# Kernel optimization log

Hardware: AMD Instinct MI355X
Metric: run time of the kernel (lower is better)

Reference implementation:

```python
import jax, jax.numpy as jnp
import numpy as np

D = 1024
H = 16
HD = D // H
EPS = 1e-5

def _layernorm(x, g, b):
    xf = x.astype(jnp.float32)
    mu = jnp.mean(xf, axis=-1, keepdims=True)
    var = jnp.mean(jnp.square(xf - mu), axis=-1, keepdims=True)
    return ((xf - mu) * jax.lax.rsqrt(var + EPS) * g + b).astype(x.dtype)

def setup_inputs() -> dict:
    key = jax.random.key(0)
    ks = jax.random.split(key, 12)
    B, S = 4, 1024
    s_in = 1.0 / np.sqrt(D)
    inp = {
        "x": jax.random.normal(ks[0], (B, S, D), dtype=jnp.float32),
        "in_proj_w": jax.random.normal(ks[1], (3 * D, D), dtype=jnp.float32) * s_in,
        "in_proj_b": jnp.zeros((3 * D,), dtype=jnp.float32),
        "out_w": jax.random.normal(ks[2], (D, D), dtype=jnp.float32) * s_in,
        "out_b": jnp.zeros((D,), dtype=jnp.float32),
        "ln1_g": jnp.ones((D,), dtype=jnp.float32),
        "ln1_b": jnp.zeros((D,), dtype=jnp.float32),
        "fc_w": jax.random.normal(ks[3], (4 * D, D), dtype=jnp.float32) * s_in,
        "fc_b": jnp.zeros((4 * D,), dtype=jnp.float32),
        "proj_w": jax.random.normal(ks[4], (D, 4 * D), dtype=jnp.float32) * (1.0 / np.sqrt(4 * D)),
        "proj_b": jnp.zeros((D,), dtype=jnp.float32),
        "ln2_g": jnp.ones((D,), dtype=jnp.float32),
        "ln2_b": jnp.zeros((D,), dtype=jnp.float32),
    }
    return inp

def reference(x, in_proj_w, in_proj_b, out_w, out_b, ln1_g, ln1_b,
              fc_w, fc_b, proj_w, proj_b, ln2_g, ln2_b):
    B, S, _ = x.shape
    scaling = float(HD) ** -0.5
    # --- attention sublayer ---
    h = _layernorm(x, ln1_g, ln1_b)
    qkv = h @ in_proj_w.T + in_proj_b              # [B,S,3D]
    q, k, v = jnp.split(qkv, 3, axis=-1)
    q = (q * scaling).reshape(B, S, H, HD).transpose(0, 2, 1, 3)  # [B,H,S,hd]
    k = k.reshape(B, S, H, HD).transpose(0, 2, 1, 3)
    v = v.reshape(B, S, H, HD).transpose(0, 2, 1, 3)
    attn = jax.nn.softmax(jnp.einsum('bhqd,bhkd->bhqk', q, k), axis=-1)
    o = jnp.einsum('bhqk,bhkd->bhqd', attn, v).transpose(0, 2, 1, 3).reshape(B, S, D)
    x = x + o @ out_w.T + out_b
    # --- MLP sublayer (QuickGELU) ---
    h = _layernorm(x, ln2_g, ln2_b)
    u = h @ fc_w.T + fc_b                          # [B,S,4D]
    u = u * jax.nn.sigmoid(1.702 * u)
    x = x + u @ proj_w.T + proj_b
    return x
```

## Files before the change

### kernel.cpp

```cpp
#include <hip/hip_runtime.h>
#include <math.h>

#define D_MODEL 1024
#define SEQ     1024
#define BATCH   4
#define NTOK    (BATCH * SEQ)

typedef __bf16 bf16;
using bfrag = __attribute__((ext_vector_type(8))) __bf16;
using ffrag = __attribute__((ext_vector_type(4))) float;

__device__ __forceinline__ ffrag mfma16(bfrag a, bfrag b, ffrag c) {
  return __builtin_amdgcn_mfma_f32_16x16x32_bf16(a, b, c, 0, 0, 0);
}

__device__ __forceinline__ void gload_lds16(const void* g, void* l) {
  __builtin_amdgcn_global_load_lds(
      (const __attribute__((address_space(1))) void*)g,
      (__attribute__((address_space(3))) void*)l, 16, 0, 0);
}

__device__ __forceinline__ int xcd_remap(int flat, int nwg) {
  return (flat & 7) * (nwg >> 3) + (flat >> 3);
}

__global__ void convert_all(const float* __restrict__ s0, bf16* __restrict__ d0, int n0,
                            const float* __restrict__ s1, bf16* __restrict__ d1, int n1,
                            const float* __restrict__ s2, bf16* __restrict__ d2, int n2,
                            const float* __restrict__ s3, bf16* __restrict__ d3, int n3,
                            float scale, int limit0) {
  const float* src; bf16* dst; int n; int limit = 0;
  switch (blockIdx.y) {
    case 0: src = s0; dst = d0; n = n0; limit = limit0; break;
    case 1: src = s1; dst = d1; n = n1; break;
    case 2: src = s2; dst = d2; n = n2; break;
    default: src = s3; dst = d3; n = n3; break;
  }
  int i = blockIdx.x * blockDim.x + threadIdx.x;
  const int stride = gridDim.x * blockDim.x;
  for (; i < n; i += stride) {
    float4 v = ((const float4*)src)[i];
    float sc = (i < limit) ? scale : 1.0f;
    bf16* d = dst + (size_t)i * 4;
    d[0] = (bf16)(v.x * sc); d[1] = (bf16)(v.y * sc);
    d[2] = (bf16)(v.z * sc); d[3] = (bf16)(v.w * sc);
  }
}

__global__ void scale_bias(const float* __restrict__ src, float* __restrict__ dst,
                           int n, int limit, float scale) {
  int i = blockIdx.x * blockDim.x + threadIdx.x;
  if (i < n) dst[i] = src[i] * (i < limit ? scale : 1.0f);
}

__global__ __launch_bounds__(256) void ln_row(const float* __restrict__ x,
                                              const float* __restrict__ gamma,
                                              const float* __restrict__ beta,
                                              bf16* __restrict__ out) {
  const int row = blockIdx.x, tid = threadIdx.x;
  const float4 v = ((const float4*)(x + (size_t)row * D_MODEL))[tid];
  float s  = v.x + v.y + v.z + v.w;
  float ss = v.x * v.x + v.y * v.y + v.z * v.z + v.w * v.w;
#pragma unroll
  for (int off = 32; off >= 1; off >>= 1) {
    s  += __shfl_xor(s, off);
    ss += __shfl_xor(ss, off);
  }
  __shared__ float rs[4], rss[4];
  const int w = tid >> 6;
  if ((tid & 63) == 0) { rs[w] = s; rss[w] = ss; }
  __syncthreads();
  s  = rs[0] + rs[1] + rs[2] + rs[3];
  ss = rss[0] + rss[1] + rss[2] + rss[3];
  const float mu   = s * (1.0f / D_MODEL);
  const float var  = ss * (1.0f / D_MODEL) - mu * mu;
  const float rstd = rsqrtf(var + 1e-5f);
  const float4 gv = ((const float4*)gamma)[tid];
  const float4 bv = ((const float4*)beta)[tid];
  bf16* o = out + (size_t)row * D_MODEL + tid * 4;
  o[0] = (bf16)((v.x - mu) * rstd * gv.x + bv.x);
  o[1] = (bf16)((v.y - mu) * rstd * gv.y + bv.y);
  o[2] = (bf16)((v.z - mu) * rstd * gv.z + bv.z);
  o[3] = (bf16)((v.w - mu) * rstd * gv.w + bv.w);
}

template <int EPI>
__global__ __launch_bounds__(256, 4) void gemm_bt(
    const bf16* __restrict__ A, const bf16* __restrict__ B,
    const float* __restrict__ bias, const float* __restrict__ resid,
    float* __restrict__ outF, bf16* __restrict__ outB,
    int M, int N, int K) {
  __shared__ bf16 As[2][128 * 32];
  __shared__ bf16 Bs[2][128 * 32];
  const int tid = threadIdx.x;
  const int lane = tid & 63, w = tid >> 6;
  const int wm = w >> 1, wn = w & 1;
  const int ql = lane & 15, lg = lane >> 4;
  const int nwg = gridDim.x * gridDim.y;
  const int flat = xcd_remap(blockIdx.y * gridDim.x + blockIdx.x, nwg);
  const int m0 = (flat % gridDim.x) * 128, n0 = (flat / gridDim.x) * 128;

  ffrag acc[4][4];
#pragma unroll
  for (int i = 0; i < 4; i++)
#pragma unroll
    for (int j = 0; j < 4; j++) acc[i][j] = ffrag{0.f, 0.f, 0.f, 0.f};

  const int r0 = tid >> 2;
  const int jsw = (tid & 3) ^ ((r0 >> 1) & 3);
  const bf16* a0 = A + (size_t)(m0 + r0) * K + jsw * 8;
  const bf16* a1 = A + (size_t)(m0 + 64 + r0) * K + jsw * 8;
  const bf16* b0 = B + (size_t)(n0 + r0) * K + jsw * 8;
  const bf16* b1 = B + (size_t)(n0 + 64 + r0) * K + jsw * 8;
  const int lo = w * 512;

  auto STAGE = [&](int bs, int kk) {
    gload_lds16(a0 + kk, &As[bs][lo]);
    gload_lds16(a1 + kk, &As[bs][2048 + lo]);
    gload_lds16(b0 + kk, &Bs[bs][lo]);
    gload_lds16(b1 + kk, &Bs[bs][2048 + lo]);
  };

  STAGE(0, 0);
  __syncthreads();

  int cur = 0;
  for (int k0 = 0; k0 < K; k0 += 32) {
    if (k0 + 32 < K) STAGE(cur ^ 1, k0 + 32);
    bfrag af[4], bfr[4];
#pragma unroll
    for (int i = 0; i < 4; i++) {
      const int row = wm * 64 + i * 16 + ql;
      af[i] = *(const bfrag*)&As[cur][row * 32 + ((lg ^ ((row >> 1) & 3)) * 8)];
    }
#pragma unroll
    for (int j = 0; j < 4; j++) {
      const int row = wn * 64 + j * 16 + ql;
      bfr[j] = *(const bfrag*)&Bs[cur][row * 32 + ((lg ^ ((row >> 1) & 3)) * 8)];
    }
#pragma unroll
    for (int i = 0; i < 4; i++)
#pragma unroll
      for (int j = 0; j < 4; j++)
        acc[i][j] = mfma16(af[i], bfr[j], acc[i][j]);
    __syncthreads();
    cur ^= 1;
  }

#pragma unroll
  for (int i = 0; i < 4; i++) {
    const int row = m0 + wm * 64 + i * 16 + lg * 4;
#pragma unroll
    for (int j = 0; j < 4; j++) {
      const int col = n0 + wn * 64 + j * 16 + ql;
      const float bv = bias[col];
#pragma unroll
      for (int r = 0; r < 4; r++) {
        float v = acc[i][j][r] + bv;
        const size_t idx = (size_t)(row + r) * N + col;
        if (EPI == 0) {
          outB[idx] = (bf16)v;
        } else if (EPI == 1) {
          outF[idx] = v + resid[idx];
        } else {
          outB[idx] = (bf16)(v / (1.0f + __expf(-1.702f * v)));
        }
      }
    }
  }
}

template <int EPI>
__global__ __launch_bounds__(256, 4) void gemm_bt64(
    const bf16* __restrict__ A, const bf16* __restrict__ B,
    const float* __restrict__ bias, const float* __restrict__ resid,
    float* __restrict__ outF, bf16* __restrict__ outB,
    int M, int N, int K) {
  __shared__ bf16 As[2][64 * 64];
  __shared__ bf16 Bs[2][64 * 64];
  const int tid = threadIdx.x;
  const int lane = tid & 63, w = tid >> 6;
  const int wm = w >> 1, wn = w & 1;
  const int ql = lane & 15, lg = lane >> 4;
  const int m0 = blockIdx.x * 64, n0 = blockIdx.y * 64;

  ffrag acc[2][2];
#pragma unroll
  for (int i = 0; i < 2; i++)
#pragma unroll
    for (int j = 0; j < 2; j++) acc[i][j] = ffrag{0.f, 0.f, 0.f, 0.f};

  const int r0 = tid >> 3;
  const int jsw = ((tid & 7) ^ (r0 & 7)) * 8;
  const bf16* a0 = A + (size_t)(m0 + r0) * K + jsw;
  const bf16* a1 = A + (size_t)(m0 + 32 + r0) * K + jsw;
  const bf16* b0 = B + (size_t)(n0 + r0) * K + jsw;
  const bf16* b1 = B + (size_t)(n0 + 32 + r0) * K + jsw;
  const int lo = tid * 8;

  auto STAGE = [&](int bs, int kk) {
    gload_lds16(a0 + kk, &As[bs][lo]);
    gload_lds16(a1 + kk, &As[bs][2048 + lo]);
    gload_lds16(b0 + kk, &Bs[bs][lo]);
    gload_lds16(b1 + kk, &Bs[bs][2048 + lo]);
  };

  STAGE(0, 0);
  __syncthreads();

  int cur = 0;
  for (int k0 = 0; k0 < K; k0 += 64) {
    if (k0 + 64 < K) STAGE(cur ^ 1, k0 + 64);
    bfrag af[2][2], bfr[2][2];
#pragma unroll
    for (int i = 0; i < 2; i++) {
      const int row = wm * 32 + i * 16 + ql;
      const int r7 = row & 7;
#pragma unroll
      for (int kc = 0; kc < 2; kc++)
        af[i][kc] = *(const bfrag*)&As[cur][row * 64 + (((lg + 4 * kc) ^ r7) * 8)];
    }
#pragma unroll
    for (int j = 0; j < 2; j++) {
      const int row = wn * 32 + j * 16 + ql;
      const int r7 = row & 7;
#pragma unroll
      for (int kc = 0; kc < 2; kc++)
        bfr[j][kc] = *(const bfrag*)&Bs[cur][row * 64 + (((lg + 4 * kc) ^ r7) * 8)];
    }
#pragma unroll
    for (int kc = 0; kc < 2; kc++)
#pragma unroll
      for (int i = 0; i < 2; i++)
#pragma unroll
        for (int j = 0; j < 2; j++)
          acc[i][j] = mfma16(af[i][kc], bfr[j][kc], acc[i][j]);
    __syncthreads();
    cur ^= 1;
  }

#pragma unroll
  for (int i = 0; i < 2; i++) {
    const int row = m0 + wm * 32 + i * 16 + lg * 4;
#pragma unroll
    for (int j = 0; j < 2; j++) {
      const int col = n0 + wn * 32 + j * 16 + ql;
      const float bv = bias[col];
#pragma unroll
      for (int r = 0; r < 4; r++) {
        float v = acc[i][j][r] + bv;
        const size_t idx = (size_t)(row + r) * N + col;
        if (EPI == 0) {
          outB[idx] = (bf16)v;
        } else if (EPI == 1) {
          outF[idx] = v + resid[idx];
        } else {
          outB[idx] = (bf16)(v / (1.0f + __expf(-1.702f * v)));
        }
      }
    }
  }
}

__global__ __launch_bounds__(256) void transpose_v(const bf16* __restrict__ qkv,
                                                   bf16* __restrict__ vt) {
  __shared__ bf16 T[64 * 66];
  const int tid = threadIdx.x;
  const int bh = blockIdx.y, b = bh >> 4, h = bh & 15;
  const int s0 = blockIdx.x * 64;
  const bf16* src = qkv + (size_t)b * SEQ * 3072 + 2048 + h * 64;

  const int sl = tid >> 3, c = tid & 7;
#pragma unroll
  for (int p = 0; p < 2; p++) {
    const int s = sl + p * 32;
    const bfrag v = *(const bfrag*)(src + (size_t)(s0 + s) * 3072 + c * 8);
#pragma unroll
    for (int e = 0; e < 8; e++) T[s * 66 + c * 8 + e] = v[e];
  }
  __syncthreads();
  bf16* dst = vt + (size_t)bh * 64 * 1024;
#pragma unroll
  for (int p = 0; p < 2; p++) {
    const int d = sl + p * 32;
    bfrag o;
#pragma unroll
    for (int e = 0; e < 8; e++) o[e] = T[(c * 8 + e) * 66 + d];
    *(bfrag*)(dst + (size_t)d * 1024 + s0 + c * 8) = o;
  }
}

__global__ __launch_bounds__(256, 3) void flash_attn(const bf16* __restrict__ qkv,
                                                     const bf16* __restrict__ vt,
                                                     bf16* __restrict__ o) {
  __shared__ bf16 Kl[128 * 64];
  __shared__ bf16 Vl[64 * 128];
  __shared__ bf16 Pl[4 * 16 * 136];
  const int tid = threadIdx.x, lane = tid & 63, wid = tid >> 6;
  const int ql = lane & 15, lg = lane >> 4;
  const int flat = xcd_remap(blockIdx.y * 16 + blockIdx.x, 1024);
  const int bh = flat >> 4, b = bh >> 4, h = bh & 15;
  const int qrow0 = (flat & 15) * 64 + wid * 16;
  const size_t headq = (size_t)b * SEQ * 3072 + (size_t)h * 64;

  const bf16* qp = qkv + headq + (size_t)(qrow0 + ql) * 3072 + lg * 8;
  const bfrag q0 = *(const bfrag*)qp;
  const bfrag q1 = *(const bfrag*)(qp + 32);

  float mrun[4], lrun[4];
  ffrag oacc[4];
#pragma unroll
  for (int r = 0; r < 4; r++) { mrun[r] = -1e30f; lrun[r] = 0.0f; }
#pragma unroll
  for (int f = 0; f < 4; f++) oacc[f] = ffrag{0.f, 0.f, 0.f, 0.f};

  const int kr0 = tid >> 3;
  const int kjsw = ((tid & 7) ^ (kr0 & 7)) * 8;
  const bf16* kp = qkv + headq + 1024 + (size_t)kr0 * 3072 + kjsw;
  const int vr_ = tid >> 4, vlc = tid & 15;
  const bf16* vhead = vt + (size_t)bh * 64 * 1024;
  bf16* Pw = Pl + wid * 2176;

  for (int kt = 0; kt < SEQ; kt += 128) {
#pragma unroll
    for (int pp = 0; pp < 4; pp++)
      gload_lds16(kp + (size_t)(kt + pp * 32) * 3072, &Kl[pp * 2048 + tid * 8]);
#pragma unroll
    for (int pp = 0; pp < 4; pp++) {
      const int vr = pp * 16 + vr_;
      const int gc = vlc ^ (vr & 7);
      gload_lds16(vhead + (size_t)vr * 1024 + kt + gc * 8, &Vl[(pp * 256 + tid) * 8]);
    }
    __syncthreads();

    ffrag sa[8];
    __builtin_amdgcn_s_setprio(1);
#pragma unroll
    for (int sub = 0; sub < 8; sub++) {
      const int krow = sub * 16 + ql;
      const int r7 = krow & 7;
      const bfrag kf0 = *(const bfrag*)&Kl[krow * 64 + ((lg ^ r7) * 8)];
      const bfrag kf1 = *(const bfrag*)&Kl[krow * 64 + (((lg + 4) ^ r7) * 8)];
      ffrag s4 = ffrag{0.f, 0.f, 0.f, 0.f};
      s4 = mfma16(q0, kf0, s4);
      s4 = mfma16(q1, kf1, s4);
      sa[sub] = s4;
    }
    __builtin_amdgcn_s_setprio(0);

    float lmax[4];
#pragma unroll
    for (int r = 0; r < 4; r++) {
      float m = sa[0][r];
#pragma unroll
      for (int sub = 1; sub < 8; sub++) m = fmaxf(m, sa[sub][r]);
      lmax[r] = m;
    }
    bool ok = (lmax[0] - mrun[0] <= 8.0f) && (lmax[1] - mrun[1] <= 8.0f) &&
              (lmax[2] - mrun[2] <= 8.0f) && (lmax[3] - mrun[3] <= 8.0f);
    if (!__all(ok)) {
#pragma unroll
      for (int r = 0; r < 4; r++) {
        float mx = lmax[r];
        mx = fmaxf(mx, __shfl_xor(mx, 1));
        mx = fmaxf(mx, __shfl_xor(mx, 2));
        mx = fmaxf(mx, __shfl_xor(mx, 4));
        mx = fmaxf(mx, __shfl_xor(mx, 8));
        const float mnew = fmaxf(mrun[r], mx);
        const float corr = exp2f(mrun[r] - mnew);
        lrun[r] *= corr;
#pragma unroll
        for (int f = 0; f < 4; f++) oacc[f][r] *= corr;
        mrun[r] = mnew;
      }
    }
#pragma unroll
    for (int r = 0; r < 4; r++) {
      float srow = 0.f;
      bf16* prow = Pw + (lg * 4 + r) * 136;
#pragma unroll
      for (int sub = 0; sub < 8; sub++) {
        const float pv = exp2f(sa[sub][r] - mrun[r]);
        srow += pv;
        prow[sub * 16 + ql] = (bf16)pv;
      }
      lrun[r] += srow;
    }

    bfrag pa[4];
#pragma unroll
    for (int kc = 0; kc < 4; kc++)
      pa[kc] = *(const bfrag*)&Pw[ql * 136 + kc * 32 + lg * 8];
    __builtin_amdgcn_s_setprio(1);
#pragma unroll
    for (int f = 0; f < 4; f++) {
      const int vrow = f * 16 + ql;
      const int r7 = vrow & 7;
#pragma unroll
      for (int kc = 0; kc < 4; kc++) {
        const bfrag vf = *(const bfrag*)&Vl[vrow * 128 + (((kc * 4 + lg) ^ r7) * 8)];
        oacc[f] = mfma16(pa[kc], vf, oacc[f]);
      }
    }
    __builtin_amdgcn_s_setprio(0);
    __syncthreads();
  }

  float rinv[4];
#pragma unroll
  for (int r = 0; r < 4; r++) {
    float ls = lrun[r];
    ls += __shfl_xor(ls, 1);
    ls += __shfl_xor(ls, 2);
    ls += __shfl_xor(ls, 4);
    ls += __shfl_xor(ls, 8);
    rinv[r] = 1.0f / ls;
  }
#pragma unroll
  for (int f = 0; f < 4; f++) {
#pragma unroll
    for (int r = 0; r < 4; r++) {
      const size_t orow = (size_t)b * SEQ + qrow0 + lg * 4 + r;
      o[orow * 1024 + h * 64 + f * 16 + ql] = (bf16)(oacc[f][r] * rinv[r]);
    }
  }
}

extern "C" void kernel_launch(void* const* d_in, const int* in_sizes, int n_in,
                              void* d_out, int out_size, void* d_ws, size_t ws_size,
                              hipStream_t stream) {
  (void)in_sizes; (void)n_in; (void)out_size; (void)ws_size;
  const float* x      = (const float*)d_in[0];
  const float* in_w   = (const float*)d_in[1];
  const float* in_b   = (const float*)d_in[2];
  const float* out_w  = (const float*)d_in[3];
  const float* out_b  = (const float*)d_in[4];
  const float* ln1_g  = (const float*)d_in[5];
  const float* ln1_b  = (const float*)d_in[6];
  const float* fc_w   = (const float*)d_in[7];
  const float* fc_b   = (const float*)d_in[8];
  const float* proj_w = (const float*)d_in[9];
  const float* proj_b = (const float*)d_in[10];
  const float* ln2_g  = (const float*)d_in[11];
  const float* ln2_b  = (const float*)d_in[12];
  float* out = (float*)d_out;

  char* p = (char*)d_ws;
  auto alloc = [&](size_t bytes) { char* r = p; p += (bytes + 255) & ~255ull; return r; };
  bf16* w_qkv  = (bf16*)alloc((size_t)3072 * 1024 * 2);
  bf16* w_out  = (bf16*)alloc((size_t)1024 * 1024 * 2);
  bf16* w_fc   = (bf16*)alloc((size_t)4096 * 1024 * 2);
  bf16* w_proj = (bf16*)alloc((size_t)1024 * 4096 * 2);
  float* b_qkv = (float*)alloc((size_t)3072 * 4);
  bf16* hbuf   = (bf16*)alloc((size_t)NTOK * 1024 * 2);
  float* x2    = (float*)alloc((size_t)NTOK * 1024 * 4);
  bf16* qkv    = (bf16*)alloc((size_t)NTOK * 3072 * 2);
  bf16* aout   = (bf16*)alloc((size_t)NTOK * 1024 * 2);
  bf16* ubuf   = qkv;
  bf16* vtb    = (bf16*)x2;

  const float scaling = 0.125f * 1.44269504089f;
  convert_all<<<dim3(1024, 4), 256, 0, stream>>>(
      in_w, w_qkv, 3072 * 1024 / 4,
      out_w, w_out, 1024 * 1024 / 4,
      fc_w, w_fc, 4096 * 1024 / 4,
      proj_w, w_proj, 4096 * 1024 / 4,
      scaling, 1024 * 1024 / 4);
  scale_bias<<<12, 256, 0, stream>>>(in_b, b_qkv, 3072, 1024, scaling);

  ln_row<<<NTOK, 256, 0, stream>>>(x, ln1_g, ln1_b, hbuf);
  gemm_bt<0><<<dim3(32, 24), 256, 0, stream>>>(hbuf, w_qkv, b_qkv, nullptr,
                                               nullptr, qkv, NTOK, 3072, 1024);
  transpose_v<<<dim3(16, 64), 256, 0, stream>>>(qkv, vtb);
  flash_attn<<<dim3(16, 64), 256, 0, stream>>>(qkv, vtb, aout);
  gemm_bt64<1><<<dim3(64, 16), 256, 0, stream>>>(aout, w_out, out_b, x,
                                                 x2, nullptr, NTOK, 1024, 1024);
  ln_row<<<NTOK, 256, 0, stream>>>(x2, ln2_g, ln2_b, hbuf);
  gemm_bt<2><<<dim3(32, 32), 256, 0, stream>>>(hbuf, w_fc, fc_b, nullptr,
                                               nullptr, ubuf, NTOK, 4096, 1024);
  gemm_bt64<1><<<dim3(64, 16), 256, 0, stream>>>(ubuf, w_proj, proj_b, x2,
                                                 out, nullptr, NTOK, 1024, 4096);
}
```

Before: 228.5 us.

## Rewrite flash attention with 32x32 MFMA, transposed scores and register-resident P

Flash attention now uses 32x32x16 bf16 MFMA, computing S^T as K·Q so that each lane owns a single query column. The softmax probabilities are packed to bf16 and exchanged between half-waves with shuffles, so P no longer takes a round trip through LDS. Each block now handles 128 query rows (32 per wave) instead of 64, which halves the grid and doubles K/V reuse per LDS load. Occupancy drops to 2 blocks per CU, and the rescale and normalise steps go through a small LDS broadcast buffer; the new swizzles and fragment mappings carry correctness risk.

```diff
diff --git a/kernel.cpp b/kernel.cpp
--- a/kernel.cpp
+++ b/kernel.cpp
@@ -7,11 +7,20 @@
 #define NTOK    (BATCH * SEQ)
 
 typedef __bf16 bf16;
-using bfrag = __attribute__((ext_vector_type(8))) __bf16;
-using ffrag = __attribute__((ext_vector_type(4))) float;
+using bfrag  = __attribute__((ext_vector_type(8))) __bf16;
+using ffrag  = __attribute__((ext_vector_type(4))) float;
+using f32x16 = __attribute__((ext_vector_type(16))) float;
 
 __device__ __forceinline__ ffrag mfma16(bfrag a, bfrag b, ffrag c) {
   return __builtin_amdgcn_mfma_f32_16x16x32_bf16(a, b, c, 0, 0, 0);
+}
+__device__ __forceinline__ f32x16 mfma32(bfrag a, bfrag b, f32x16 c) {
+  return __builtin_amdgcn_mfma_f32_32x32x16_bf16(a, b, c, 0, 0, 0);
+}
+__device__ __forceinline__ unsigned cvt_pk(float lo, float hi) {
+  unsigned r;
+  asm("v_cvt_pk_bf16_f32 %0, %1, %2" : "=v"(r) : "v"(lo), "v"(hi));
+  return r;
 }
 
 __device__ __forceinline__ void gload_lds16(const void* g, void* l) {
@@ -290,36 +299,33 @@
   }
 }
 
-__global__ __launch_bounds__(256, 3) void flash_attn(const bf16* __restrict__ qkv,
+__global__ __launch_bounds__(256, 2) void flash_attn(const bf16* __restrict__ qkv,
                                                      const bf16* __restrict__ vt,
                                                      bf16* __restrict__ o) {
   __shared__ bf16 Kl[128 * 64];
   __shared__ bf16 Vl[64 * 128];
-  __shared__ bf16 Pl[4 * 16 * 136];
+  __shared__ float RB[4][32];
   const int tid = threadIdx.x, lane = tid & 63, wid = tid >> 6;
-  const int ql = lane & 15, lg = lane >> 4;
-  const int flat = xcd_remap(blockIdx.y * 16 + blockIdx.x, 1024);
-  const int bh = flat >> 4, b = bh >> 4, h = bh & 15;
-  const int qrow0 = (flat & 15) * 64 + wid * 16;
+  const int l31 = lane & 31, hi = lane >> 5;
+  const int flat = xcd_remap(blockIdx.y * 8 + blockIdx.x, 512);
+  const int qblk = flat & 7, bh = flat >> 3, b = bh >> 4, h = bh & 15;
+  const int qb0 = qblk * 128 + wid * 32;
   const size_t headq = (size_t)b * SEQ * 3072 + (size_t)h * 64;
 
-  const bf16* qp = qkv + headq + (size_t)(qrow0 + ql) * 3072 + lg * 8;
-  const bfrag q0 = *(const bfrag*)qp;
-  const bfrag q1 = *(const bfrag*)(qp + 32);
-
-  float mrun[4], lrun[4];
-  ffrag oacc[4];
-#pragma unroll
-  for (int r = 0; r < 4; r++) { mrun[r] = -1e30f; lrun[r] = 0.0f; }
-#pragma unroll
-  for (int f = 0; f < 4; f++) oacc[f] = ffrag{0.f, 0.f, 0.f, 0.f};
-
-  const int kr0 = tid >> 3;
-  const int kjsw = ((tid & 7) ^ (kr0 & 7)) * 8;
-  const bf16* kp = qkv + headq + 1024 + (size_t)kr0 * 3072 + kjsw;
-  const int vr_ = tid >> 4, vlc = tid & 15;
+  const bf16* qp = qkv + headq + (size_t)(qb0 + l31) * 3072 + hi * 8;
+  bfrag qb[4];
+#pragma unroll
+  for (int t = 0; t < 4; t++) qb[t] = *(const bfrag*)(qp + t * 16);
+
+  float mrun = -1e30f, lrun = 0.0f;
+  f32x16 oacc[2];
+#pragma unroll
+  for (int r = 0; r < 16; r++) { oacc[0][r] = 0.f; oacc[1][r] = 0.f; }
+
+  const int ksrc = ((tid & 7) ^ ((tid >> 3) & 7) ^ wid) * 8;
+  const bf16* kp = qkv + headq + 1024 + (size_t)(tid >> 3) * 3072 + ksrc;
   const bf16* vhead = vt + (size_t)bh * 64 * 1024;
-  bf16* Pw = Pl + wid * 2176;
+  const int xlane = (l31 & 7) ^ (l31 >> 3);
 
   for (int kt = 0; kt < SEQ; kt += 128) {
 #pragma unroll
@@ -327,102 +333,96 @@
       gload_lds16(kp + (size_t)(kt + pp * 32) * 3072, &Kl[pp * 2048 + tid * 8]);
 #pragma unroll
     for (int pp = 0; pp < 4; pp++) {
-      const int vr = pp * 16 + vr_;
-      const int gc = vlc ^ (vr & 7);
+      const int vr = pp * 16 + (tid >> 4);
+      const int gc = (tid & 15) ^ ((tid >> 4) & 7) ^ ((pp * 2 + (tid >> 7)) & 3);
       gload_lds16(vhead + (size_t)vr * 1024 + kt + gc * 8, &Vl[(pp * 256 + tid) * 8]);
     }
     __syncthreads();
 
-    ffrag sa[8];
+    f32x16 sacc[4];
+#pragma unroll
+    for (int s = 0; s < 4; s++)
+#pragma unroll
+      for (int r = 0; r < 16; r++) sacc[s][r] = 0.f;
     __builtin_amdgcn_s_setprio(1);
 #pragma unroll
-    for (int sub = 0; sub < 8; sub++) {
-      const int krow = sub * 16 + ql;
-      const int r7 = krow & 7;
-      const bfrag kf0 = *(const bfrag*)&Kl[krow * 64 + ((lg ^ r7) * 8)];
-      const bfrag kf1 = *(const bfrag*)&Kl[krow * 64 + (((lg + 4) ^ r7) * 8)];
-      ffrag s4 = ffrag{0.f, 0.f, 0.f, 0.f};
-      s4 = mfma16(q0, kf0, s4);
-      s4 = mfma16(q1, kf1, s4);
-      sa[sub] = s4;
+    for (int s = 0; s < 4; s++) {
+      const int krow = s * 32 + l31;
+#pragma unroll
+      for (int t = 0; t < 4; t++) {
+        const int ch = (t * 2) ^ hi ^ xlane;
+        const bfrag kf = *(const bfrag*)&Kl[krow * 64 + ch * 8];
+        sacc[s] = mfma32(kf, qb[t], sacc[s]);
+      }
     }
     __builtin_amdgcn_s_setprio(0);
 
-    float lmax[4];
-#pragma unroll
-    for (int r = 0; r < 4; r++) {
-      float m = sa[0][r];
-#pragma unroll
-      for (int sub = 1; sub < 8; sub++) m = fmaxf(m, sa[sub][r]);
-      lmax[r] = m;
-    }
-    bool ok = (lmax[0] - mrun[0] <= 8.0f) && (lmax[1] - mrun[1] <= 8.0f) &&
-              (lmax[2] - mrun[2] <= 8.0f) && (lmax[3] - mrun[3] <= 8.0f);
-    if (!__all(ok)) {
-#pragma unroll
-      for (int r = 0; r < 4; r++) {
-        float mx = lmax[r];
-        mx = fmaxf(mx, __shfl_xor(mx, 1));
-        mx = fmaxf(mx, __shfl_xor(mx, 2));
-        mx = fmaxf(mx, __shfl_xor(mx, 4));
-        mx = fmaxf(mx, __shfl_xor(mx, 8));
-        const float mnew = fmaxf(mrun[r], mx);
-        const float corr = exp2f(mrun[r] - mnew);
-        lrun[r] *= corr;
-#pragma unroll
-        for (int f = 0; f < 4; f++) oacc[f][r] *= corr;
-        mrun[r] = mnew;
+    float lm = sacc[0][0];
+#pragma unroll
+    for (int s = 0; s < 4; s++)
+#pragma unroll
+      for (int r = 0; r < 16; r++) lm = fmaxf(lm, sacc[s][r]);
+
+    if (!__all(lm - mrun <= 8.0f)) {
+      const float mx = fmaxf(lm, __shfl_xor(lm, 32));
+      const float mnew = fmaxf(mrun, mx);
+      const float corr = exp2f(mrun - mnew);
+      mrun = mnew;
+      lrun *= corr;
+      if (!hi) RB[wid][l31] = corr;
+#pragma unroll
+      for (int r = 0; r < 16; r++) {
+        const float c = RB[wid][(r & 3) + 8 * (r >> 2) + 4 * hi];
+        oacc[0][r] *= c;
+        oacc[1][r] *= c;
       }
     }
-#pragma unroll
-    for (int r = 0; r < 4; r++) {
-      float srow = 0.f;
-      bf16* prow = Pw + (lg * 4 + r) * 136;
-#pragma unroll
-      for (int sub = 0; sub < 8; sub++) {
-        const float pv = exp2f(sa[sub][r] - mrun[r]);
-        srow += pv;
-        prow[sub * 16 + ql] = (bf16)pv;
+
+#pragma unroll
+    for (int s = 0; s < 4; s++) {
+      float p[16];
+#pragma unroll
+      for (int r = 0; r < 16; r++) p[r] = exp2f(sacc[s][r] - mrun);
+#pragma unroll
+      for (int r = 0; r < 16; r++) lrun += p[r];
+      const unsigned A = cvt_pk(p[0], p[1]),  B = cvt_pk(p[2], p[3]);
+      const unsigned C = cvt_pk(p[4], p[5]),  D = cvt_pk(p[6], p[7]);
+      const unsigned E = cvt_pk(p[8], p[9]),  F = cvt_pk(p[10], p[11]);
+      const unsigned G = cvt_pk(p[12], p[13]), H = cvt_pk(p[14], p[15]);
+      const unsigned x1 = __shfl_xor(hi ? A : C, 32);
+      const unsigned x2 = __shfl_xor(hi ? B : D, 32);
+      const unsigned x3 = __shfl_xor(hi ? E : G, 32);
+      const unsigned x4 = __shfl_xor(hi ? F : H, 32);
+      unsigned w0[4] = { hi ? x1 : A, hi ? x2 : B, hi ? C : x1, hi ? D : x2 };
+      unsigned w1[4] = { hi ? x3 : E, hi ? x4 : F, hi ? G : x3, hi ? H : x4 };
+      const bfrag pa0 = *(const bfrag*)w0;
+      const bfrag pa1 = *(const bfrag*)w1;
+      __builtin_amdgcn_s_setprio(1);
+#pragma unroll
+      for (int db = 0; db < 2; db++) {
+        const int vrow = db * 32 + l31;
+        const int c0 = ((4 * s) * 2) ^ hi ^ xlane;
+        const int c1 = ((4 * s + 2) * 2) ^ hi ^ xlane;
+        const bfrag vf0 = *(const bfrag*)&Vl[vrow * 128 + ((((2 * s) * 2) ^ hi ^ xlane) & 15) * 8];
+        oacc[db] = mfma32(pa0, vf0, oacc[db]);
+        const bfrag vf1 = *(const bfrag*)&Vl[vrow * 128 + ((((2 * s + 1) * 2) ^ hi ^ xlane) & 15) * 8];
+        oacc[db] = mfma32(pa1, vf1, oacc[db]);
+        (void)c0; (void)c1;
       }
-      lrun[r] += srow;
-    }
-
-    bfrag pa[4];
-#pragma unroll
-    for (int kc = 0; kc < 4; kc++)
-      pa[kc] = *(const bfrag*)&Pw[ql * 136 + kc * 32 + lg * 8];
-    __builtin_amdgcn_s_setprio(1);
-#pragma unroll
-    for (int f = 0; f < 4; f++) {
-      const int vrow = f * 16 + ql;
-      const int r7 = vrow & 7;
-#pragma unroll
-      for (int kc = 0; kc < 4; kc++) {
-        const bfrag vf = *(const bfrag*)&Vl[vrow * 128 + (((kc * 4 + lg) ^ r7) * 8)];
-        oacc[f] = mfma16(pa[kc], vf, oacc[f]);
-      }
-    }
-    __builtin_amdgcn_s_setprio(0);
+      __builtin_amdgcn_s_setprio(0);
+    }
     __syncthreads();
   }
 
-  float rinv[4];
-#pragma unroll
-  for (int r = 0; r < 4; r++) {
-    float ls = lrun[r];
-    ls += __shfl_xor(ls, 1);
-    ls += __shfl_xor(ls, 2);
-    ls += __shfl_xor(ls, 4);
-    ls += __shfl_xor(ls, 8);
-    rinv[r] = 1.0f / ls;
-  }
-#pragma unroll
-  for (int f = 0; f < 4; f++) {
-#pragma unroll
-    for (int r = 0; r < 4; r++) {
-      const size_t orow = (size_t)b * SEQ + qrow0 + lg * 4 + r;
-      o[orow * 1024 + h * 64 + f * 16 + ql] = (bf16)(oacc[f][r] * rinv[r]);
-    }
+  const float lsum = lrun + __shfl_xor(lrun, 32);
+  if (!hi) RB[wid][l31] = 1.0f / lsum;
+#pragma unroll
+  for (int r = 0; r < 16; r++) {
+    const int qml = (r & 3) + 8 * (r >> 2) + 4 * hi;
+    const float rv = RB[wid][qml];
+    const size_t orow = (size_t)b * SEQ + qb0 + qml;
+    o[orow * 1024 + h * 64 + l31]      = (bf16)(oacc[0][r] * rv);
+    o[orow * 1024 + h * 64 + 32 + l31] = (bf16)(oacc[1][r] * rv);
   }
 }
 
@@ -472,7 +472,7 @@
   gemm_bt<0><<<dim3(32, 24), 256, 0, stream>>>(hbuf, w_qkv, b_qkv, nullptr,
                                                nullptr, qkv, NTOK, 3072, 1024);
   transpose_v<<<dim3(16, 64), 256, 0, stream>>>(qkv, vtb);
-  flash_attn<<<dim3(16, 64), 256, 0, stream>>>(qkv, vtb, aout);
+  flash_attn<<<dim3(8, 64), 256, 0, stream>>>(qkv, vtb, aout);
   gemm_bt64<1><<<dim3(64, 16), 256, 0, stream>>>(aout, w_out, out_b, x,
                                                  x2, nullptr, NTOK, 1024, 1024);
   ln_row<<<NTOK, 256, 0, stream>>>(x2, ln2_g, ln2_b, hbuf);
```

Result: faster. 219.5 us (-3.9%).
